# Kernel tuning notes

Hardware: AMD Instinct MI355X
Metric: run time of the kernel (lower is better)

Reference implementation:

```python
import jax, jax.numpy as jnp
import numpy as np

NUM_EXPERTS = 8
NUM_LANGS = 4
TOP_K = 2
D_MODEL = 1024
EXPERT_SIZE = 4096
B, S = 2, 2048


def setup_inputs() -> dict:
    key = jax.random.key(0)
    ks = jax.random.split(key, 6)
    def xavier(k, shape, fan_in, fan_out):
        a = float(np.sqrt(6.0 / (fan_in + fan_out)))
        return jax.random.uniform(k, shape, jnp.float32, -a, a)
    return {
        "x": jax.random.normal(ks[0], (B, S, D_MODEL), jnp.float32),
        "router_w": xavier(ks[1], (NUM_EXPERTS, D_MODEL), D_MODEL, NUM_EXPERTS),
        "router_b": jnp.zeros((NUM_EXPERTS,), jnp.float32),
        "lang_w": xavier(ks[2], (NUM_LANGS, D_MODEL), D_MODEL, NUM_LANGS),
        "lang_b": jnp.zeros((NUM_LANGS,), jnp.float32),
        "w1": xavier(ks[3], (NUM_EXPERTS, D_MODEL, EXPERT_SIZE), D_MODEL, EXPERT_SIZE),
        "b1": jnp.zeros((NUM_EXPERTS, EXPERT_SIZE), jnp.float32),
        "w2": xavier(ks[4], (NUM_EXPERTS, EXPERT_SIZE, D_MODEL), EXPERT_SIZE, D_MODEL),
        "b2": jnp.zeros((NUM_EXPERTS, D_MODEL), jnp.float32),
    }


def reference(x, router_w, router_b, lang_w, lang_b, w1, b1, w2, b2):
    # Language-aware routing bias
    lang_logits = x @ lang_w.T + lang_b                      # [B,S,L]
    lang_probs = jax.nn.softmax(lang_logits, axis=-1)
    # lang_probs[..., idx:idx+2].sum(-1): slice may be width 1 at the edge,
    # emulate with a zero pad column.
    lp_pad = jnp.pad(lang_probs, ((0, 0), (0, 0), (0, 1)))
    idx = jnp.arange(NUM_EXPERTS) % NUM_LANGS                # [E]
    expert_weights = lp_pad[..., idx] + lp_pad[..., idx + 1] # [B,S,E]

    router_logits = x @ router_w.T + router_b + 0.1 * expert_weights
    router_probs = jax.nn.softmax(router_logits, axis=-1)   # [B,S,E]
    top_p, top_i = jax.lax.top_k(router_probs, TOP_K)        # [B,S,K]
    top_p = top_p / top_p.sum(axis=-1, keepdims=True)

    # Dense per-expert MLP (dropout=0 / eval). torch GELU default = exact erf.
    h = jax.nn.gelu(jnp.einsum('bsd,edh->bseh', x, w1) + b1, approximate=False)
    expert_out = jnp.einsum('bseh,ehd->bsed', h, w2) + b2    # [B,S,E,D]

    sel = jnp.take_along_axis(expert_out, top_i[..., None], axis=2)  # [B,S,K,D]
    return (top_p[..., None] * sel).sum(axis=2)              # [B,S,D]
```

## Files before the change

### kernel.cpp

```cpp
#include <hip/hip_runtime.h>
#include <cstdint>
#include <cstddef>

#define T_TOK 4096
#define DM 1024
#define HS 4096
#define NE 8
#define MAXROWS 9216
#define MAXTILES 72

typedef __attribute__((ext_vector_type(8))) short short8;
typedef __attribute__((ext_vector_type(4))) float floatx4;

__device__ __forceinline__ unsigned short f2bf(float f) {
  union { float f; unsigned u; } v; v.f = f;
  unsigned r = (v.u + 0x7fffu + ((v.u >> 16) & 1u)) >> 16;
  return (unsigned short)r;
}

__device__ __forceinline__ void gload_lds16(const void* g, void* l) {
  __builtin_amdgcn_global_load_lds((const __attribute__((address_space(1))) void*)g,
                                   (__attribute__((address_space(3))) void*)l, 16, 0, 0);
}


__global__ void k_cvt_init(const float* __restrict__ x, unsigned short* __restrict__ xb,
                           int* counts, int* cursor, unsigned* list) {
  int i = blockIdx.x * 256 + threadIdx.x;
  if (i < NE) { counts[i] = 0; cursor[i] = 0; }
  if (i < MAXROWS) list[i] = 0xFFFFFFFFu;
  float4 v = ((const float4*)x)[i];
  union { unsigned short us[4]; uint2 u2; } o;
  o.us[0] = f2bf(v.x); o.us[1] = f2bf(v.y); o.us[2] = f2bf(v.z); o.us[3] = f2bf(v.w);
  ((uint2*)xb)[i] = o.u2;
}

__global__ void k_route(const float* __restrict__ x, const float* __restrict__ rw,
                        const float* __restrict__ rb, const float* __restrict__ lw,
                        const float* __restrict__ lb, int* __restrict__ top_i,
                        float* __restrict__ top_p, int* __restrict__ counts) {
  int t = blockIdx.x * 4 + (threadIdx.x >> 6);
  int lane = threadIdx.x & 63;
  const float4* xt = (const float4*)(x + (size_t)t * DM);
  float4 xv[4];
#pragma unroll
  for (int j = 0; j < 4; j++) xv[j] = xt[lane * 4 + j];
  float dots[12];
#pragma unroll
  for (int r = 0; r < 12; r++) {
    const float4* wr = (const float4*)(r < 4 ? lw + r * DM : rw + (r - 4) * DM);
    float s = 0.f;
#pragma unroll
    for (int j = 0; j < 4; j++) {
      float4 w = wr[lane * 4 + j];
      s += xv[j].x * w.x + xv[j].y * w.y + xv[j].z * w.z + xv[j].w * w.w;
    }
#pragma unroll
    for (int o = 32; o > 0; o >>= 1) s += __shfl_xor(s, o, 64);
    dots[r] = s;
  }
  if (lane == 0) {
    float lp[4]; float m = -1e30f;
#pragma unroll
    for (int i = 0; i < 4; i++) { lp[i] = dots[i] + lb[i]; m = fmaxf(m, lp[i]); }
    float sum = 0.f;
#pragma unroll
    for (int i = 0; i < 4; i++) { lp[i] = expf(lp[i] - m); sum += lp[i]; }
#pragma unroll
    for (int i = 0; i < 4; i++) lp[i] /= sum;
    float ew[4];
    ew[0] = lp[0] + lp[1]; ew[1] = lp[1] + lp[2]; ew[2] = lp[2] + lp[3]; ew[3] = lp[3];
    float r8[8];
#pragma unroll
    for (int e = 0; e < 8; e++) r8[e] = dots[4 + e] + rb[e] + 0.1f * ew[e & 3];
    int e0 = 0;
#pragma unroll
    for (int e = 1; e < 8; e++) if (r8[e] > r8[e0]) e0 = e;
    int e1 = (e0 == 0) ? 1 : 0;
#pragma unroll
    for (int e = 0; e < 8; e++) if (e != e0 && r8[e] > r8[e1]) e1 = e;
    float tt = expf(r8[e1] - r8[e0]);
    float w0 = 1.f / (1.f + tt);
    float w1 = tt / (1.f + tt);
    top_i[t * 2] = e0; top_i[t * 2 + 1] = e1;
    top_p[t * 2] = w0; top_p[t * 2 + 1] = w1;
    atomicAdd(&counts[e0], 1); atomicAdd(&counts[e1], 1);
  }
}

__global__ void k_offsets(const int* counts, int* off) {
  if (threadIdx.x == 0) {
    int acc = 0;
    for (int e = 0; e < NE; e++) {
      off[e] = acc;
      int p = ((counts[e] + 127) >> 7) << 7;
      acc += p;
    }
    off[NE] = acc;
  }
}

__global__ void k_scatter(const int* __restrict__ top_i, const int* __restrict__ off,
                          int* cursor, unsigned* __restrict__ list) {
  int t = blockIdx.x * 256 + threadIdx.x;
  if (t >= T_TOK) return;
#pragma unroll
  for (int k = 0; k < 2; k++) {
    int e = top_i[t * 2 + k];
    int pos = atomicAdd(&cursor[e], 1);
    list[off[e] + pos] = (unsigned)(t * 2 + k);
  }
}

__global__ void k_transpose_bf16(const float* __restrict__ src, unsigned short* __restrict__ dst,
                                 int K, int N) {
  __shared__ float tile[64][65];
  const float* s = src + (size_t)blockIdx.z * K * N;
  unsigned short* d = dst + (size_t)blockIdx.z * K * N;
  int n0 = blockIdx.x * 64, k0 = blockIdx.y * 64;
  int tr = threadIdx.x >> 4;
  int tc = (threadIdx.x & 15) * 4;
#pragma unroll
  for (int j = 0; j < 4; j++) {
    int row = tr + j * 16;
    float4 v = *(const float4*)&s[(size_t)(k0 + row) * N + n0 + tc];
    tile[row][tc + 0] = v.x; tile[row][tc + 1] = v.y;
    tile[row][tc + 2] = v.z; tile[row][tc + 3] = v.w;
  }
  __syncthreads();
#pragma unroll
  for (int j = 0; j < 4; j++) {
    int n = tr + j * 16;
    union { unsigned short us[4]; uint2 u2; } o;
#pragma unroll
    for (int i = 0; i < 4; i++) o.us[i] = f2bf(tile[tc + i][n]);
    *(uint2*)&d[(size_t)(n0 + n) * K + k0 + tc] = o.u2;
  }
}

__global__ void k_init_out(const int* __restrict__ top_i, const float* __restrict__ top_p,
                           const float* __restrict__ b2, float* __restrict__ out) {
  int i = blockIdx.x * 256 + threadIdx.x;
  int t = i >> 10, d = i & 1023;
  int e0 = top_i[t * 2], e1 = top_i[t * 2 + 1];
  out[i] = top_p[t * 2] * b2[e0 * DM + d] + top_p[t * 2 + 1] * b2[e1 * DM + d];
}

template <int MODE, int K, int N, int KT>
__global__ __launch_bounds__(256, 3) void k_gemm(
    const unsigned short* __restrict__ Abase,
    const unsigned short* __restrict__ Wt,
    const int* __restrict__ off, const unsigned* __restrict__ list,
    const float* __restrict__ bias, const float* __restrict__ top_p,
    unsigned short* __restrict__ Hout, float* __restrict__ out) {
  int gx = gridDim.x, gy = gridDim.y;
  int flat = (blockIdx.z * gy + blockIdx.y) * gx + blockIdx.x;
  int nwg = gx * gy * gridDim.z;
  int cpx = nwg >> 3;
  int swz = (flat & 7) * cpx + (flat >> 3);
  int bn = swz % gx; int rest = swz / gx;
  int bm = rest % gy; int zz = rest / gy;
  int n0 = bn * 128;
  int r0 = bm * 128;
  int kb = zz * (KT * 32);

  int total = off[NE];
  if (r0 >= total) return;
  int e = 0;
  while (r0 >= off[e + 1]) ++e;

  __shared__ __align__(16) unsigned short lA[3][128 * 32];
  __shared__ __align__(16) unsigned short lB[3][128 * 32];
  __shared__ float sP[128];
  __shared__ int sTok[128];

  int tid = threadIdx.x;
  int srow = tid >> 2;
  int skey = (srow >> 1) & 3;
  int koff_src = ((tid & 3) ^ skey) * 8;
  int ldst = srow * 32 + (tid & 3) * 8;

  const unsigned short* srcA[2];
#pragma unroll
  for (int c = 0; c < 2; c++) {
    int row = c * 64 + srow;
    size_t arow;
    if (MODE == 0) {
      unsigned pair = list[r0 + row];
      arow = (pair == 0xFFFFFFFFu) ? 0 : (size_t)(pair >> 1);
    } else {
      arow = (size_t)(r0 + row);
    }
    srcA[c] = Abase + arow * K + kb + koff_src;
  }
  const unsigned short* srcB[2];
#pragma unroll
  for (int c = 0; c < 2; c++)
    srcB[c] = Wt + ((size_t)e * N + n0 + c * 64 + srow) * K + kb + koff_src;

  if (MODE == 1 && tid < 128) {
    unsigned pair = list[r0 + tid];
    if (pair == 0xFFFFFFFFu) { sTok[tid] = -1; sP[tid] = 0.f; }
    else { sTok[tid] = (int)(pair >> 1); sP[tid] = top_p[pair]; }
  }

  floatx4 acc[4][4] = {};
  int lane = tid & 63;
  int w = tid >> 6;
  int wm = w >> 1, wn = w & 1;
  int lr = lane & 15, kq = lane >> 4;
  int kx = kq ^ ((lr >> 1) & 3);
  int aBase = (wm * 64 + lr) * 4 + kx;
  int bBase = (wn * 64 + lr) * 4 + kx;

#define STAGE_A(BUF, TT)                                                      \
  do {                                                                        \
    _Pragma("unroll")                                                         \
    for (int c = 0; c < 2; c++)                                               \
      gload_lds16(srcA[c] + (size_t)(TT) * 32, &lA[BUF][c * 2048 + ldst]);    \
  } while (0)
#define STAGE_B(BUF, TT)                                                      \
  do {                                                                        \
    _Pragma("unroll")                                                         \
    for (int c = 0; c < 2; c++)                                               \
      gload_lds16(srcB[c] + (size_t)(TT) * 32, &lB[BUF][c * 2048 + ldst]);    \
  } while (0)

  __syncthreads();

  STAGE_A(0, 0); STAGE_B(0, 0);
  STAGE_A(1, 1); STAGE_B(1, 1);
  asm volatile("s_waitcnt vmcnt(4)\ns_barrier" ::: "memory");

  int cur = 0, nxt = 2;
  for (int t = 0; t < KT; ++t) {
    const short8* pA = (const short8*)lA[cur];
    const short8* pB = (const short8*)lB[cur];
    bool pf = (t + 2 < KT);
    if (pf) STAGE_A(nxt, t + 2);
    short8 a0[4], b0[2];
#pragma unroll
    for (int m = 0; m < 4; m++) a0[m] = pA[aBase + m * 64];
#pragma unroll
    for (int n = 0; n < 2; n++) b0[n] = pB[bBase + n * 64];
    __builtin_amdgcn_s_setprio(1);
#pragma unroll
    for (int m = 0; m < 4; m++)
#pragma unroll
      for (int n = 0; n < 2; n++)
        acc[m][n] = __builtin_amdgcn_mfma_f32_16x16x32_bf16(a0[m], b0[n], acc[m][n], 0, 0, 0);
    __builtin_amdgcn_s_setprio(0);
    if (pf) STAGE_B(nxt, t + 2);
    short8 b1v[2];
#pragma unroll
    for (int n = 0; n < 2; n++) b1v[n] = pB[bBase + (n + 2) * 64];
    __builtin_amdgcn_s_setprio(1);
#pragma unroll
    for (int m = 0; m < 4; m++)
#pragma unroll
      for (int n = 0; n < 2; n++)
        acc[m][n + 2] = __builtin_amdgcn_mfma_f32_16x16x32_bf16(a0[m], b1v[n], acc[m][n + 2], 0, 0, 0);
    __builtin_amdgcn_s_setprio(0);
    if (t + 1 < KT) {
      if (pf) asm volatile("s_waitcnt vmcnt(4)\ns_barrier" ::: "memory");
      else    asm volatile("s_waitcnt vmcnt(0)\ns_barrier" ::: "memory");
    }
    cur = (cur == 2) ? 0 : cur + 1;
    nxt = (nxt == 2) ? 0 : nxt + 1;
  }
#undef STAGE_A
#undef STAGE_B

  int rbase = wm * 64 + kq * 4;
  int cbase = wn * 64 + lr;
  if (MODE == 0) {
#pragma unroll
    for (int i = 0; i < 4; i++)
#pragma unroll
      for (int j = 0; j < 4; j++)
#pragma unroll
        for (int g = 0; g < 4; g++) {
          int row = rbase + i * 16 + g;
          int col = cbase + j * 16;
          float v = acc[i][j][g] + bias[e * N + n0 + col];
          float u = v * (0.7978845608f + 0.0356774081f * v * v);
          float gl = v / (1.f + __expf(-2.f * u));
          Hout[(size_t)(r0 + row) * (size_t)N + n0 + col] = f2bf(gl);
        }
  } else {
#pragma unroll
    for (int i = 0; i < 4; i++)
#pragma unroll
      for (int j = 0; j < 4; j++)
#pragma unroll
        for (int g = 0; g < 4; g++) {
          int row = rbase + i * 16 + g;
          int col = cbase + j * 16;
          int tok = sTok[row];
          if (tok >= 0)
            atomicAdd(&out[(size_t)tok * DM + n0 + col], sP[row] * acc[i][j][g]);
        }
  }
}


extern "C" void kernel_launch(void* const* d_in, const int* in_sizes, int n_in,
                              void* d_out, int out_size, void* d_ws, size_t ws_size,
                              hipStream_t stream) {
  const float* x  = (const float*)d_in[0];
  const float* rw = (const float*)d_in[1];
  const float* rb = (const float*)d_in[2];
  const float* lw = (const float*)d_in[3];
  const float* lb = (const float*)d_in[4];
  const float* w1 = (const float*)d_in[5];
  const float* b1 = (const float*)d_in[6];
  const float* w2 = (const float*)d_in[7];
  const float* b2 = (const float*)d_in[8];
  float* out = (float*)d_out;
  char* ws = (char*)d_ws;

  int* counts = (int*)ws;
  int* cursor = (int*)(ws + 32);
  int* off    = (int*)(ws + 64);
  int* top_i  = (int*)(ws + 128);
  float* top_p = (float*)(ws + 128 + 32768);
  unsigned* list = (unsigned*)(ws + 65792);
  unsigned short* xb = (unsigned short*)(ws + 102912);
  unsigned short* wt = (unsigned short*)(ws + 102912 + 8388608);
  unsigned short* h  = (unsigned short*)(ws + 102912 + 8388608 + 67108864);

  k_cvt_init<<<dim3(T_TOK * DM / 4 / 256), dim3(256), 0, stream>>>(x, xb, counts, cursor, list);
  k_route<<<dim3(T_TOK / 4), dim3(256), 0, stream>>>(x, rw, rb, lw, lb, top_i, top_p, counts);
  k_offsets<<<dim3(1), dim3(64), 0, stream>>>(counts, off);
  k_scatter<<<dim3(T_TOK / 256), dim3(256), 0, stream>>>(top_i, off, cursor, list);
  k_transpose_bf16<<<dim3(HS / 64, DM / 64, NE), dim3(256), 0, stream>>>(w1, wt, DM, HS);
  k_init_out<<<dim3(T_TOK * DM / 256), dim3(256), 0, stream>>>(top_i, top_p, b2, out);
  k_gemm<0, DM, HS, DM / 32><<<dim3(HS / 128, MAXTILES, 1), dim3(256), 0, stream>>>(
      xb, wt, off, list, b1, top_p, h, nullptr);
  k_transpose_bf16<<<dim3(DM / 64, HS / 64, NE), dim3(256), 0, stream>>>(w2, wt, HS, DM);
  k_gemm<1, HS, DM, HS / 4 / 32><<<dim3(DM / 128, MAXTILES, 4), dim3(256), 0, stream>>>(
      h, wt, off, list, nullptr, top_p, nullptr, out);
}
```

Baseline: 541.5 us.

## Enlarge grouped GEMM tiles to 256x256x64 with 512-thread double-buffered pipeline

Reworks both expert GEMMs to use 256x256 output tiles with K-step 64, 512-thread workgroups (8 waves each computing 128x64), and a two-stage LDS buffer in place of the three-stage 128x128x32 design. Expert segments are padded to 256 rows, and the maximum tile count and workspace offsets change to match. The aim is more MFMA work per LDS load and less global traffic per FLOP. The cost is more padding rows, much lower occupancy (one block per CU, large register and LDS footprint), fewer workgroups, and a full vmcnt(0) wait plus barrier on every iteration.

```diff
diff --git a/kernel.cpp b/kernel.cpp
--- a/kernel.cpp
+++ b/kernel.cpp
@@ -6,8 +6,8 @@
 #define DM 1024
 #define HS 4096
 #define NE 8
-#define MAXROWS 9216
-#define MAXTILES 72
+#define MAXROWS 10240
+#define MAXTILES 40
 
 typedef __attribute__((ext_vector_type(8))) short short8;
 typedef __attribute__((ext_vector_type(4))) float floatx4;
@@ -93,7 +93,7 @@
     int acc = 0;
     for (int e = 0; e < NE; e++) {
       off[e] = acc;
-      int p = ((counts[e] + 127) >> 7) << 7;
+      int p = ((counts[e] + 255) >> 8) << 8;
       acc += p;
     }
     off[NE] = acc;
@@ -147,7 +147,7 @@
 }
 
 template <int MODE, int K, int N, int KT>
-__global__ __launch_bounds__(256, 3) void k_gemm(
+__global__ __launch_bounds__(512, 1) void k_gemm(
     const unsigned short* __restrict__ Abase,
     const unsigned short* __restrict__ Wt,
     const int* __restrict__ off, const unsigned* __restrict__ list,
@@ -159,147 +159,139 @@
   int cpx = nwg >> 3;
   int swz = (flat & 7) * cpx + (flat >> 3);
   int bn = swz % gx; int rest = swz / gx;
-  int bm = rest % gy; int zz = rest / gy;
-  int n0 = bn * 128;
-  int r0 = bm * 128;
-  int kb = zz * (KT * 32);
-
+  int bm = rest % gy; int z = rest / gy;
+  int n0 = bn * 256, r0 = bm * 256;
+  int kb = z * (KT * 64);
   int total = off[NE];
   if (r0 >= total) return;
   int e = 0;
   while (r0 >= off[e + 1]) ++e;
 
-  __shared__ __align__(16) unsigned short lA[3][128 * 32];
-  __shared__ __align__(16) unsigned short lB[3][128 * 32];
-  __shared__ float sP[128];
-  __shared__ int sTok[128];
+  __shared__ __align__(16) unsigned short lA[2][256 * 64];
+  __shared__ __align__(16) unsigned short lB[2][256 * 64];
+  __shared__ float sP[256];
+  __shared__ int sTok[256];
 
   int tid = threadIdx.x;
-  int srow = tid >> 2;
-  int skey = (srow >> 1) & 3;
-  int koff_src = ((tid & 3) ^ skey) * 8;
-  int ldst = srow * 32 + (tid & 3) * 8;
-
-  const unsigned short* srcA[2];
-#pragma unroll
-  for (int c = 0; c < 2; c++) {
-    int row = c * 64 + srow;
-    size_t arow;
+  int w = tid >> 6, lane = tid & 63;
+  int g8 = lane >> 3, c8 = lane & 7;
+  int rowS = w * 8 + g8;
+  int koff = (c8 ^ g8) * 8;
+
+  unsigned aOff[4], bOff[4];
+#pragma unroll
+  for (int l = 0; l < 4; l++) {
+    int rowA = l * 64 + rowS;
+    unsigned arow;
     if (MODE == 0) {
-      unsigned pair = list[r0 + row];
-      arow = (pair == 0xFFFFFFFFu) ? 0 : (size_t)(pair >> 1);
+      unsigned pair = list[r0 + rowA];
+      arow = (pair == 0xFFFFFFFFu) ? 0u : (pair >> 1);
     } else {
-      arow = (size_t)(r0 + row);
+      arow = (unsigned)(r0 + rowA);
     }
-    srcA[c] = Abase + arow * K + kb + koff_src;
-  }
-  const unsigned short* srcB[2];
-#pragma unroll
-  for (int c = 0; c < 2; c++)
-    srcB[c] = Wt + ((size_t)e * N + n0 + c * 64 + srow) * K + kb + koff_src;
-
-  if (MODE == 1 && tid < 128) {
+    aOff[l] = arow * (unsigned)K + (unsigned)(kb + koff);
+    bOff[l] = (unsigned)(e * N + n0 + rowA) * (unsigned)K + (unsigned)(kb + koff);
+  }
+  int ldsb = rowS * 64 + c8 * 8;
+
+  if (MODE == 1 && tid < 256) {
     unsigned pair = list[r0 + tid];
     if (pair == 0xFFFFFFFFu) { sTok[tid] = -1; sP[tid] = 0.f; }
     else { sTok[tid] = (int)(pair >> 1); sP[tid] = top_p[pair]; }
   }
 
-  floatx4 acc[4][4] = {};
-  int lane = tid & 63;
-  int w = tid >> 6;
-  int wm = w >> 1, wn = w & 1;
+  int wm = w >> 2, wn = w & 3;
   int lr = lane & 15, kq = lane >> 4;
-  int kx = kq ^ ((lr >> 1) & 3);
-  int aBase = (wm * 64 + lr) * 4 + kx;
-  int bBase = (wn * 64 + lr) * 4 + kx;
-
-#define STAGE_A(BUF, TT)                                                      \
+  int rsel = (lr & 7);
+
+  floatx4 acc[8][4] = {};
+
+#define STAGE(BUF, TT)                                                        \
   do {                                                                        \
     _Pragma("unroll")                                                         \
-    for (int c = 0; c < 2; c++)                                               \
-      gload_lds16(srcA[c] + (size_t)(TT) * 32, &lA[BUF][c * 2048 + ldst]);    \
+    for (int l = 0; l < 4; l++)                                               \
+      gload_lds16(Abase + aOff[l] + (TT) * 64, &lA[BUF][l * 4096 + ldsb]);    \
+    _Pragma("unroll")                                                         \
+    for (int l = 0; l < 4; l++)                                               \
+      gload_lds16(Wt + bOff[l] + (TT) * 64, &lB[BUF][l * 4096 + ldsb]);       \
   } while (0)
-#define STAGE_B(BUF, TT)                                                      \
-  do {                                                                        \
-    _Pragma("unroll")                                                         \
-    for (int c = 0; c < 2; c++)                                               \
-      gload_lds16(srcB[c] + (size_t)(TT) * 32, &lB[BUF][c * 2048 + ldst]);    \
-  } while (0)
 
   __syncthreads();
-
-  STAGE_A(0, 0); STAGE_B(0, 0);
-  STAGE_A(1, 1); STAGE_B(1, 1);
-  asm volatile("s_waitcnt vmcnt(4)\ns_barrier" ::: "memory");
-
-  int cur = 0, nxt = 2;
+  STAGE(0, 0);
+  asm volatile("s_waitcnt vmcnt(0)" ::: "memory");
+  __builtin_amdgcn_s_barrier();
+
+  int cur = 0;
   for (int t = 0; t < KT; ++t) {
-    const short8* pA = (const short8*)lA[cur];
-    const short8* pB = (const short8*)lB[cur];
-    bool pf = (t + 2 < KT);
-    if (pf) STAGE_A(nxt, t + 2);
-    short8 a0[4], b0[2];
-#pragma unroll
-    for (int m = 0; m < 4; m++) a0[m] = pA[aBase + m * 64];
-#pragma unroll
-    for (int n = 0; n < 2; n++) b0[n] = pB[bBase + n * 64];
+    const short8* qA = (const short8*)lA[cur];
+    const short8* qB = (const short8*)lB[cur];
+    short8 a[8], b[4];
+#pragma unroll
+    for (int m = 0; m < 8; m++)
+      a[m] = qA[(wm * 128 + m * 16 + lr) * 8 + ((0 * 4 + kq) ^ rsel)];
+#pragma unroll
+    for (int n = 0; n < 4; n++)
+      b[n] = qB[(wn * 64 + n * 16 + lr) * 8 + ((0 * 4 + kq) ^ rsel)];
+    if (t + 1 < KT) STAGE(cur ^ 1, t + 1);
     __builtin_amdgcn_s_setprio(1);
 #pragma unroll
-    for (int m = 0; m < 4; m++)
-#pragma unroll
-      for (int n = 0; n < 2; n++)
-        acc[m][n] = __builtin_amdgcn_mfma_f32_16x16x32_bf16(a0[m], b0[n], acc[m][n], 0, 0, 0);
+    for (int m = 0; m < 8; m++)
+#pragma unroll
+      for (int n = 0; n < 4; n++)
+        acc[m][n] = __builtin_amdgcn_mfma_f32_16x16x32_bf16(a[m], b[n], acc[m][n], 0, 0, 0);
     __builtin_amdgcn_s_setprio(0);
-    if (pf) STAGE_B(nxt, t + 2);
-    short8 b1v[2];
-#pragma unroll
-    for (int n = 0; n < 2; n++) b1v[n] = pB[bBase + (n + 2) * 64];
+#pragma unroll
+    for (int m = 0; m < 8; m++)
+      a[m] = qA[(wm * 128 + m * 16 + lr) * 8 + ((1 * 4 + kq) ^ rsel)];
+#pragma unroll
+    for (int n = 0; n < 4; n++)
+      b[n] = qB[(wn * 64 + n * 16 + lr) * 8 + ((1 * 4 + kq) ^ rsel)];
     __builtin_amdgcn_s_setprio(1);
 #pragma unroll
-    for (int m = 0; m < 4; m++)
-#pragma unroll
-      for (int n = 0; n < 2; n++)
-        acc[m][n + 2] = __builtin_amdgcn_mfma_f32_16x16x32_bf16(a0[m], b1v[n], acc[m][n + 2], 0, 0, 0);
+    for (int m = 0; m < 8; m++)
+#pragma unroll
+      for (int n = 0; n < 4; n++)
+        acc[m][n] = __builtin_amdgcn_mfma_f32_16x16x32_bf16(a[m], b[n], acc[m][n], 0, 0, 0);
     __builtin_amdgcn_s_setprio(0);
-    if (t + 1 < KT) {
-      if (pf) asm volatile("s_waitcnt vmcnt(4)\ns_barrier" ::: "memory");
-      else    asm volatile("s_waitcnt vmcnt(0)\ns_barrier" ::: "memory");
-    }
-    cur = (cur == 2) ? 0 : cur + 1;
-    nxt = (nxt == 2) ? 0 : nxt + 1;
-  }
-#undef STAGE_A
-#undef STAGE_B
-
-  int rbase = wm * 64 + kq * 4;
-  int cbase = wn * 64 + lr;
+    asm volatile("s_waitcnt vmcnt(0)" ::: "memory");
+    __builtin_amdgcn_s_barrier();
+    cur ^= 1;
+  }
+#undef STAGE
+
   if (MODE == 0) {
-#pragma unroll
-    for (int i = 0; i < 4; i++)
-#pragma unroll
-      for (int j = 0; j < 4; j++)
+    float bcol[4];
+#pragma unroll
+    for (int n = 0; n < 4; n++) bcol[n] = bias[e * N + n0 + wn * 64 + n * 16 + lr];
+#pragma unroll
+    for (int m = 0; m < 8; m++)
+#pragma unroll
+      for (int n = 0; n < 4; n++)
 #pragma unroll
         for (int g = 0; g < 4; g++) {
-          int row = rbase + i * 16 + g;
-          int col = cbase + j * 16;
-          float v = acc[i][j][g] + bias[e * N + n0 + col];
+          int row = wm * 128 + m * 16 + kq * 4 + g;
+          int col = wn * 64 + n * 16 + lr;
+          float v = acc[m][n][g] + bcol[n];
           float u = v * (0.7978845608f + 0.0356774081f * v * v);
           float gl = v / (1.f + __expf(-2.f * u));
           Hout[(size_t)(r0 + row) * (size_t)N + n0 + col] = f2bf(gl);
         }
   } else {
 #pragma unroll
-    for (int i = 0; i < 4; i++)
-#pragma unroll
-      for (int j = 0; j < 4; j++)
-#pragma unroll
-        for (int g = 0; g < 4; g++) {
-          int row = rbase + i * 16 + g;
-          int col = cbase + j * 16;
-          int tok = sTok[row];
-          if (tok >= 0)
-            atomicAdd(&out[(size_t)tok * DM + n0 + col], sP[row] * acc[i][j][g]);
+    for (int m = 0; m < 8; m++)
+#pragma unroll
+      for (int g = 0; g < 4; g++) {
+        int row = wm * 128 + m * 16 + kq * 4 + g;
+        int tok = sTok[row];
+        if (tok >= 0) {
+          float p = sP[row];
+#pragma unroll
+          for (int n = 0; n < 4; n++) {
+            int col = wn * 64 + n * 16 + lr;
+            atomicAdd(&out[(size_t)tok * DM + n0 + col], p * acc[m][n][g]);
+          }
         }
+      }
   }
 }
 
@@ -324,10 +316,10 @@
   int* off    = (int*)(ws + 64);
   int* top_i  = (int*)(ws + 128);
   float* top_p = (float*)(ws + 128 + 32768);
-  unsigned* list = (unsigned*)(ws + 65792);
-  unsigned short* xb = (unsigned short*)(ws + 102912);
-  unsigned short* wt = (unsigned short*)(ws + 102912 + 8388608);
-  unsigned short* h  = (unsigned short*)(ws + 102912 + 8388608 + 67108864);
+  unsigned* list = (unsigned*)(ws + 128 + 65536);
+  unsigned short* xb = (unsigned short*)(ws + 131072);
+  unsigned short* wt = (unsigned short*)(ws + 131072 + 8388608);
+  unsigned short* h  = (unsigned short*)(ws + 131072 + 8388608 + 67108864);
 
   k_cvt_init<<<dim3(T_TOK * DM / 4 / 256), dim3(256), 0, stream>>>(x, xb, counts, cursor, list);
   k_route<<<dim3(T_TOK / 4), dim3(256), 0, stream>>>(x, rw, rb, lw, lb, top_i, top_p, counts);
@@ -335,9 +327,9 @@
   k_scatter<<<dim3(T_TOK / 256), dim3(256), 0, stream>>>(top_i, off, cursor, list);
   k_transpose_bf16<<<dim3(HS / 64, DM / 64, NE), dim3(256), 0, stream>>>(w1, wt, DM, HS);
   k_init_out<<<dim3(T_TOK * DM / 256), dim3(256), 0, stream>>>(top_i, top_p, b2, out);
-  k_gemm<0, DM, HS, DM / 32><<<dim3(HS / 128, MAXTILES, 1), dim3(256), 0, stream>>>(
+  k_gemm<0, DM, HS, DM / 64><<<dim3(HS / 256, MAXTILES, 1), dim3(512), 0, stream>>>(
       xb, wt, off, list, b1, top_p, h, nullptr);
   k_transpose_bf16<<<dim3(DM / 64, HS / 64, NE), dim3(256), 0, stream>>>(w2, wt, HS, DM);
-  k_gemm<1, HS, DM, HS / 4 / 32><<<dim3(DM / 128, MAXTILES, 4), dim3(256), 0, stream>>>(
+  k_gemm<1, HS, DM, HS / 4 / 64><<<dim3(DM / 256, MAXTILES, 4), dim3(512), 0, stream>>>(
       h, wt, off, list, nullptr, top_p, nullptr, out);
 }
```

After: 531.2 us. Within noise of the previous version (-1.9%).
